# Performance work log

Hardware: AMD Instinct MI355X
Metric: run time of the kernel (lower is better)

Reference implementation:

```python
import jax, jax.numpy as jnp
import numpy as np

K_CONV = 4
NUM_HEADS = 16
NUM_KV_HEADS = 8
D_HEAD = 128
ROPE_THETA = 10000.0
EPS = 1e-6
NEG_INF = -1e30


def canon_b(x, w):
    """Canon-B: causal depthwise conv1d (kernel K_CONV) with residual.
    x: [B, S, C], w: [C, K_CONV]. out[t] = x[t] + sum_k w[:,k] * x[t-k]."""
    S = x.shape[1]
    xp = jnp.pad(x, ((0, 0), (K_CONV - 1, 0), (0, 0)))
    conv = sum(xp[:, K_CONV - 1 - k:K_CONV - 1 - k + S, :] * w[:, k] for k in range(K_CONV))
    return x + conv


def rms_norm(x, w):
    var = jnp.mean(x * x, axis=-1, keepdims=True)
    return x * jax.lax.rsqrt(var + EPS) * w


def rope_cos_sin(S, d):
    inv_freq = 1.0 / (ROPE_THETA ** (jnp.arange(0, d, 2, dtype=jnp.float32) / d))
    freqs = jnp.arange(S, dtype=jnp.float32)[:, None] * inv_freq  # [S, d/2]
    emb = jnp.concatenate([freqs, freqs], axis=-1)  # [S, d]
    return jnp.cos(emb), jnp.sin(emb)


def rotate_half(x):
    x1, x2 = jnp.split(x, 2, axis=-1)
    return jnp.concatenate([-x2, x1], axis=-1)


def setup_inputs() -> dict:
    key = jax.random.key(0)
    ks = jax.random.split(key, 8)
    B, S, D = 2, 2048, 2048
    Dkv = NUM_KV_HEADS * D_HEAD
    s = 0.02
    return {
        "hidden_states": jax.random.normal(ks[0], (B, S, D), jnp.float32),
        "Wq": jax.random.normal(ks[1], (D, D), jnp.float32) * s,
        "Wk": jax.random.normal(ks[2], (Dkv, D), jnp.float32) * s,
        "Wv": jax.random.normal(ks[3], (Dkv, D), jnp.float32) * s,
        "Wo": jax.random.normal(ks[4], (D, D), jnp.float32) * s,
        "canon_q_w": jax.random.normal(ks[5], (D, K_CONV), jnp.float32) * 0.1,
        "canon_k_w": jax.random.normal(ks[6], (Dkv, K_CONV), jnp.float32) * 0.1,
        "canon_v_w": jax.random.normal(ks[7], (Dkv, K_CONV), jnp.float32) * 0.1,
        "q_norm_w": jnp.ones((D_HEAD,), jnp.float32),
        "k_norm_w": jnp.ones((D_HEAD,), jnp.float32),
    }


def reference(hidden_states, Wq, Wk, Wv, Wo, canon_q_w, canon_k_w, canon_v_w, q_norm_w, k_norm_w):
    B, S, D = hidden_states.shape
    scale = 1.0 / np.sqrt(D_HEAD)
    groups = NUM_HEADS // NUM_KV_HEADS

    # QKV projections (no bias)
    q = hidden_states @ Wq.T
    k = hidden_states @ Wk.T
    v = hidden_states @ Wv.T

    # Canon-B causal depthwise conv on flat projections
    q = canon_b(q, canon_q_w)
    k = canon_b(k, canon_k_w)
    v = canon_b(v, canon_v_w)

    # Split heads: [B, S, H, d_head]
    q = q.reshape(B, S, NUM_HEADS, D_HEAD)
    k = k.reshape(B, S, NUM_KV_HEADS, D_HEAD)
    v = v.reshape(B, S, NUM_KV_HEADS, D_HEAD)

    # qk RMSNorm over d_head
    q = rms_norm(q, q_norm_w)
    k = rms_norm(k, k_norm_w)

    # RoPE
    cos, sin = rope_cos_sin(S, D_HEAD)  # [S, d_head]
    cos = cos[None, :, None, :]
    sin = sin[None, :, None, :]
    q = q * cos + rotate_half(q) * sin
    k = k * cos + rotate_half(k) * sin

    # [B, H, S, d_head]
    q = q.transpose(0, 2, 1, 3)
    k = k.transpose(0, 2, 1, 3)
    v = v.transpose(0, 2, 1, 3)

    # GQA: repeat kv heads
    k = jnp.repeat(k, groups, axis=1)
    v = jnp.repeat(v, groups, axis=1)

    # Causal attention (eager)
    scores = jnp.einsum("bhqd,bhkd->bhqk", q, k) * scale
    causal = jnp.tril(jnp.ones((S, S), bool))
    scores = jnp.where(causal, scores, NEG_INF)
    probs = jax.nn.softmax(scores, axis=-1)
    attn = jnp.einsum("bhqk,bhkd->bhqd", probs, v)

    out = attn.transpose(0, 2, 1, 3).reshape(B, S, D)
    return out @ Wo.T
```

## Files before the change

### kernel.cpp

```cpp
#include <hip/hip_runtime.h>
#include <hip/hip_bf16.h>

typedef __bf16 bf16;
typedef __bf16 bf16x8 __attribute__((ext_vector_type(8)));
typedef float  floatx4 __attribute__((ext_vector_type(4)));

#define AS1 __attribute__((address_space(1)))
#define AS3 __attribute__((address_space(3)))

#define B_    2
#define S_    2048
#define D_    2048
#define H_    16
#define KVH_  8
#define DH_   128
#define M_    4096
#define NQKV_ 4096

__global__ __launch_bounds__(256) void prep_kernel(const float* __restrict__ hidden,
                                                   const float* __restrict__ Wq,
                                                   const float* __restrict__ Wk,
                                                   const float* __restrict__ Wv,
                                                   const float* __restrict__ Wo,
                                                   bf16* __restrict__ X,
                                                   bf16* __restrict__ Wcat,
                                                   bf16* __restrict__ Wob,
                                                   float* __restrict__ cost,
                                                   float* __restrict__ sint) {
    size_t u = (size_t)blockIdx.x * 256 + threadIdx.x;
    if (u < 5242880) {
        const float* src; bf16* dst; size_t off;
        if (u < 2097152)      { src = hidden; dst = X;              off = u; }
        else if (u < 3145728) { src = Wq;     dst = Wcat;           off = u - 2097152; }
        else if (u < 3670016) { src = Wk;     dst = Wcat + 4194304; off = u - 3145728; }
        else if (u < 4194304) { src = Wv;     dst = Wcat + 6291456; off = u - 3670016; }
        else                  { src = Wo;     dst = Wob;            off = u - 4194304; }
        float4 v = *(const float4*)(src + off * 4);
        union { bf16 h[4]; double d; } uu;
        uu.h[0] = (bf16)v.x; uu.h[1] = (bf16)v.y; uu.h[2] = (bf16)v.z; uu.h[3] = (bf16)v.w;
        *(double*)(dst + off * 4) = uu.d;
    } else {
        int r = (int)(u - 5242880);
        int t = r >> 6, fi = r & 63;
        float inv = expf(-9.210340371976184f * (float)fi * (1.0f / 64.0f));
        float ang = (float)t * inv;
        cost[r] = cosf(ang);
        sint[r] = sinf(ang);
    }
}

#define BM 128
#define BN 128
#define BK 64
template <typename CT>
__global__ __launch_bounds__(256) void gemm_bt(const bf16* __restrict__ A,
                                               const bf16* __restrict__ Bw,
                                               CT* __restrict__ C,
                                               int M, int N, int K) {
    __shared__ __align__(16) bf16 Als[BM * BK];
    __shared__ __align__(16) bf16 Bls[BN * BK];
    int tid  = threadIdx.x;
    int wave = tid >> 6, lane = tid & 63;
    int quad = lane >> 4, l16 = lane & 15;
    int wm = (wave >> 1) << 6;
    int wn = (wave & 1) << 6;

    long bm0 = (long)blockIdx.y * BM;
    long bn0 = (long)blockIdx.x * BN;
    const bf16* Ab = A  + bm0 * K;
    const bf16* Bb = Bw + bn0 * K;

    int srow = wave * 32 + (lane >> 3);
    int scol = ((lane & 7) ^ (lane >> 3)) << 3;
    int sdst = (wave * 32 + (lane >> 3)) * BK + ((lane & 7) << 3);

    floatx4 acc[4][4] = {};

    for (int k0 = 0; k0 < K; k0 += BK) {
        #pragma unroll
        for (int i = 0; i < 4; ++i) {
            const bf16* ga = Ab + (long)(srow + i * 8) * K + k0 + scol;
            const bf16* gb = Bb + (long)(srow + i * 8) * K + k0 + scol;
            __builtin_amdgcn_global_load_lds((AS1 const unsigned int*)ga,
                                             (AS3 unsigned int*)(Als + sdst + i * 512), 16, 0, 0);
            __builtin_amdgcn_global_load_lds((AS1 const unsigned int*)gb,
                                             (AS3 unsigned int*)(Bls + sdst + i * 512), 16, 0, 0);
        }
        __syncthreads();
        #pragma unroll
        for (int ks = 0; ks < 2; ++ks) {
            bf16x8 af[4], bfr[4];
            #pragma unroll
            for (int t = 0; t < 4; ++t) {
                int row = wm + t * 16 + l16;
                int g = (ks * 4 + quad) ^ (row & 7);
                af[t] = *(const bf16x8*)(Als + row * BK + (g << 3));
            }
            #pragma unroll
            for (int t = 0; t < 4; ++t) {
                int row = wn + t * 16 + l16;
                int g = (ks * 4 + quad) ^ (row & 7);
                bfr[t] = *(const bf16x8*)(Bls + row * BK + (g << 3));
            }
            #pragma unroll
            for (int mt = 0; mt < 4; ++mt)
                #pragma unroll
                for (int nt = 0; nt < 4; ++nt)
                    acc[mt][nt] = __builtin_amdgcn_mfma_f32_16x16x32_bf16(af[mt], bfr[nt], acc[mt][nt], 0, 0, 0);
        }
        __syncthreads();
    }
    #pragma unroll
    for (int mt = 0; mt < 4; ++mt) {
        #pragma unroll
        for (int nt = 0; nt < 4; ++nt) {
            long row = bm0 + wm + mt * 16 + quad * 4;
            long col = bn0 + wn + nt * 16 + l16;
            #pragma unroll
            for (int r = 0; r < 4; ++r)
                C[(row + r) * N + col] = (CT)acc[mt][nt][r];
        }
    }
}

__global__ __launch_bounds__(256, 4) void canon_kernel(const bf16* __restrict__ QKV,
                                                       const float* __restrict__ wq,
                                                       const float* __restrict__ wk,
                                                       const float* __restrict__ wv,
                                                       const float* __restrict__ qnw,
                                                       const float* __restrict__ knw,
                                                       const float* __restrict__ cost,
                                                       const float* __restrict__ sint,
                                                       bf16* __restrict__ qf,
                                                       bf16* __restrict__ kf,
                                                       bf16* __restrict__ vfrag) {
    __shared__ __align__(16) bf16 vtile[32 * 520];
    int tid  = threadIdx.x;
    int wid  = blockIdx.x * 4 + (tid >> 6);
    int lane = tid & 63;
    int b  = wid >> 11;
    int g  = (wid >> 8) & 7;
    int c  = wid & 255;
    int t0 = c << 3;
    int ch = (g << 9) + (lane << 3);

    const float* wrow; int cw;
    if (g < 4)      { wrow = wq; cw = ch; }
    else if (g < 6) { wrow = wk; cw = ch - 2048; }
    else            { wrow = wv; cw = ch - 3072; }

    float4 w4[8];
    #pragma unroll
    for (int j = 0; j < 8; ++j) w4[j] = *(const float4*)(wrow + (cw + j) * 4);

    union U8 { float4 v; bf16 h[8]; };
    const bf16* srcb = QKV + (size_t)((b << 11) + t0) * 4096 + ch;

    float xm1[8], xm2[8], xm3[8];
    if (t0 > 0) {
        U8 u1, u2, u3;
        u1.v = *(const float4*)(srcb - 4096);
        u2.v = *(const float4*)(srcb - 2 * 4096);
        u3.v = *(const float4*)(srcb - 3 * 4096);
        #pragma unroll
        for (int i = 0; i < 8; ++i) {
            xm1[i] = (float)u1.h[i]; xm2[i] = (float)u2.h[i]; xm3[i] = (float)u3.h[i];
        }
    } else {
        #pragma unroll
        for (int i = 0; i < 8; ++i) { xm1[i] = 0.f; xm2[i] = 0.f; xm3[i] = 0.f; }
    }

    float4 nxtv = *(const float4*)(srcb);

    if (g < 6) {
        int j0   = ch & 127;
        int head = (g < 4) ? (ch >> 7) : ((ch - 2048) >> 7);
        const float* nw = (g < 4) ? qnw : knw;
        float nwv[8];
        {
            float4 na = *(const float4*)(nw + j0);
            float4 nb = *(const float4*)(nw + j0 + 4);
            #pragma unroll
            for (int i = 0; i < 8; ++i) nwv[i] = (i < 4) ? (&na.x)[i] : (&nb.x)[i - 4];
        }
        int ks = (lane >> 2) & 3, qd = lane & 3;
        size_t qkbase = ((size_t)((g < 4 ? (b << 4) : (b << 3)) + head) << 18)
                      + ((size_t)(t0 >> 4) << 11) + ((size_t)ks << 9)
                      + ((size_t)qd << 7) + ((size_t)(t0 & 15) << 3);
        bf16* dstb = (g < 4 ? qf : kf) + qkbase;

        int fi0 = j0 & 63;
        bool neg = (j0 < 64);
        const float* ctp = cost + t0 * 64 + fi0;
        const float* stp = sint + t0 * 64 + fi0;

        #pragma unroll
        for (int tt = 0; tt < 8; ++tt) {
            U8 u; u.v = nxtv;
            if (tt < 7) nxtv = *(const float4*)(srcb + (size_t)(tt + 1) * 4096);
            float cur[8], cv[8];
            #pragma unroll
            for (int i = 0; i < 8; ++i) cur[i] = (float)u.h[i];
            #pragma unroll
            for (int i = 0; i < 8; ++i) {
                float a = fmaf(w4[i].x, cur[i], cur[i]);
                a = fmaf(w4[i].y, xm1[i], a);
                a = fmaf(w4[i].z, xm2[i], a);
                cv[i] = fmaf(w4[i].w, xm3[i], a);
                xm3[i] = xm2[i]; xm2[i] = xm1[i]; xm1[i] = cur[i];
            }
            float ss = 0.f;
            #pragma unroll
            for (int i = 0; i < 8; ++i) ss = fmaf(cv[i], cv[i], ss);
            ss += __shfl_xor(ss, 1); ss += __shfl_xor(ss, 2);
            ss += __shfl_xor(ss, 4); ss += __shfl_xor(ss, 8);
            float r1 = rsqrtf(ss * (1.0f / 128.0f) + 1e-6f);
            float xn[8];
            #pragma unroll
            for (int i = 0; i < 8; ++i) xn[i] = cv[i] * r1 * nwv[i];
            float4 ca = *(const float4*)(ctp + tt * 64);
            float4 cb = *(const float4*)(ctp + tt * 64 + 4);
            float4 sa = *(const float4*)(stp + tt * 64);
            float4 sb = *(const float4*)(stp + tt * 64 + 4);
            __align__(16) bf16 outv[8];
            #pragma unroll
            for (int i = 0; i < 8; ++i) {
                float xp  = __shfl_xor(xn[i], 8);
                float rot = neg ? -xp : xp;
                float cc = (i < 4) ? (&ca.x)[i] : (&cb.x)[i - 4];
                float sn = (i < 4) ? (&sa.x)[i] : (&sb.x)[i - 4];
                outv[i] = (bf16)fmaf(xn[i], cc, rot * sn);
            }
            *(float4*)(dstb + (tt << 3)) = *(const float4*)outv;
        }
    } else {
        int lrow0 = (tid >> 6) << 3;
        #pragma unroll
        for (int tt = 0; tt < 8; ++tt) {
            U8 u; u.v = nxtv;
            if (tt < 7) nxtv = *(const float4*)(srcb + (size_t)(tt + 1) * 4096);
            float cur[8];
            __align__(16) bf16 outv[8];
            #pragma unroll
            for (int i = 0; i < 8; ++i) cur[i] = (float)u.h[i];
            #pragma unroll
            for (int i = 0; i < 8; ++i) {
                float a = fmaf(w4[i].x, cur[i], cur[i]);
                a = fmaf(w4[i].y, xm1[i], a);
                a = fmaf(w4[i].z, xm2[i], a);
                a = fmaf(w4[i].w, xm3[i], a);
                xm3[i] = xm2[i]; xm2[i] = xm1[i]; xm1[i] = cur[i];
                outv[i] = (bf16)a;
            }
            *(float4*)(&vtile[(lrow0 + tt) * 520 + (lane << 3)]) = *(const float4*)outv;
        }
        __syncthreads();
        int T  = (((blockIdx.x * 4) & 255) << 3);
        int kt = T >> 6, ks = (T >> 5) & 1;
        int hb = (g - 6) << 2;
        #pragma unroll
        for (int p = 0; p < 8; ++p) {
            int cidx = tid + p * 256;
            int hd  = cidx >> 9;
            int dnt = (cidx >> 6) & 7;
            int lc  = cidx & 63;
            int quad = lc >> 4, l16 = lc & 15;
            int scol = hd * 128 + dnt * 16 + l16;
            __align__(16) bf16 outv[8];
            #pragma unroll
            for (int j = 0; j < 8; ++j)
                outv[j] = vtile[(quad * 8 + j) * 520 + scol];
            size_t off = (((size_t)(b * 8 + hb + hd) * 32 + kt) << 13)
                       + ((size_t)ks << 12) + ((size_t)dnt << 9) + ((size_t)lc << 3);
            *(float4*)(vfrag + off) = *(const float4*)outv;
        }
    }
}

__global__ __launch_bounds__(256) void flash_attn(const bf16* __restrict__ qf,
                                                  const bf16* __restrict__ kf,
                                                  const bf16* __restrict__ vfrag,
                                                  bf16* __restrict__ attn) {
    __shared__ __align__(16) bf16 Kls[2][8192];
    __shared__ __align__(16) bf16 Vls[2][8192];
    __shared__ __align__(16) bf16 Pls[4][16][72];
    int lid  = blockIdx.x;
    int pair = lid & 15;
    int b    = pair >> 3, kvh = pair & 7;
    int inner = lid >> 4;
    int qt   = 31 - (inner >> 1);
    int h    = kvh * 2 + (inner & 1);
    int tid = threadIdx.x, wave = tid >> 6, lane = tid & 63;
    int quad = lane >> 4, l16 = lane & 15;
    int qrow0 = (qt << 6) + (wave << 4);

    const bf16* kfp = kf    + (((size_t)b * KVH_ + kvh) << 18);
    const bf16* vfp = vfrag + (((size_t)b * KVH_ + kvh) << 18);
    const bf16* qfp = qf    + ((((size_t)(b * H_ + h) * 128 + (qt << 2) + wave)) << 11);

    bf16x8 aq[4];
    #pragma unroll
    for (int ks = 0; ks < 4; ++ks)
        aq[ks] = *(const bf16x8*)(qfp + (ks << 9) + (lane << 3));

    floatx4 o[8] = {};
    float l_i[4] = {0.f, 0.f, 0.f, 0.f};
    const float scl2 = 0.08838834764831845f * 1.4426950408889634f;

    int ktiles = qt + 1;
    int eo = tid << 3;

    #pragma unroll
    for (int i = 0; i < 4; ++i) {
        __builtin_amdgcn_global_load_lds((AS1 const unsigned int*)(kfp + eo + (i << 11)),
                                         (AS3 unsigned int*)(&Kls[0][0] + eo + (i << 11)), 16, 0, 0);
        __builtin_amdgcn_global_load_lds((AS1 const unsigned int*)(vfp + eo + (i << 11)),
                                         (AS3 unsigned int*)(&Vls[0][0] + eo + (i << 11)), 16, 0, 0);
    }

    int cur = 0;
    for (int kt = 0; kt < ktiles; ++kt) {
        __syncthreads();
        if (kt + 1 < ktiles) {
            const bf16* ksrc = kfp + (((size_t)(kt + 1)) << 13) + eo;
            const bf16* vsrc = vfp + (((size_t)(kt + 1)) << 13) + eo;
            bf16* kd = &Kls[cur ^ 1][0] + eo;
            bf16* vd = &Vls[cur ^ 1][0] + eo;
            #pragma unroll
            for (int i = 0; i < 4; ++i) {
                __builtin_amdgcn_global_load_lds((AS1 const unsigned int*)(ksrc + (i << 11)),
                                                 (AS3 unsigned int*)(kd + (i << 11)), 16, 0, 0);
                __builtin_amdgcn_global_load_lds((AS1 const unsigned int*)(vsrc + (i << 11)),
                                                 (AS3 unsigned int*)(vd + (i << 11)), 16, 0, 0);
            }
        }
        const bf16* Kb = &Kls[cur][0];
        const bf16* Vb = &Vls[cur][0];
        floatx4 sc[4] = {};
        #pragma unroll
        for (int nt = 0; nt < 4; ++nt) {
            #pragma unroll
            for (int ks = 0; ks < 4; ++ks) {
                bf16x8 kb8 = *(const bf16x8*)(Kb + ((nt * 4 + ks) << 9) + (lane << 3));
                sc[nt] = __builtin_amdgcn_mfma_f32_16x16x32_bf16(aq[ks], kb8, sc[nt], 0, 0, 0);
            }
        }
        int qr0 = qrow0 + (quad << 2);
        int kb = kt << 6;
        if (kt == ktiles - 1) {
            #pragma unroll
            for (int nt = 0; nt < 4; ++nt) {
                int key = kb + nt * 16 + l16;
                #pragma unroll
                for (int r = 0; r < 4; ++r) {
                    float pv = exp2f(sc[nt][r] * scl2);
                    pv = (key <= qr0 + r) ? pv : 0.f;
                    l_i[r] += pv;
                    Pls[wave][(quad << 2) + r][nt * 16 + l16] = (bf16)pv;
                }
            }
        } else {
            #pragma unroll
            for (int nt = 0; nt < 4; ++nt) {
                #pragma unroll
                for (int r = 0; r < 4; ++r) {
                    float pv = exp2f(sc[nt][r] * scl2);
                    l_i[r] += pv;
                    Pls[wave][(quad << 2) + r][nt * 16 + l16] = (bf16)pv;
                }
            }
        }
        {
            bf16x8 pa = *(const bf16x8*)(&Pls[wave][l16][(quad << 3)]);
            #pragma unroll
            for (int dnt = 0; dnt < 8; ++dnt) {
                bf16x8 vb = *(const bf16x8*)(Vb + ((size_t)dnt << 9) + (lane << 3));
                o[dnt] = __builtin_amdgcn_mfma_f32_16x16x32_bf16(pa, vb, o[dnt], 0, 0, 0);
            }
            bf16x8 pb = *(const bf16x8*)(&Pls[wave][l16][32 + (quad << 3)]);
            #pragma unroll
            for (int dnt = 0; dnt < 8; ++dnt) {
                bf16x8 vb = *(const bf16x8*)(Vb + ((size_t)(8 + dnt) << 9) + (lane << 3));
                o[dnt] = __builtin_amdgcn_mfma_f32_16x16x32_bf16(pb, vb, o[dnt], 0, 0, 0);
            }
        }
        cur ^= 1;
    }
    #pragma unroll
    for (int r = 0; r < 4; ++r) {
        float l = l_i[r];
        l += __shfl_xor(l, 1); l += __shfl_xor(l, 2);
        l += __shfl_xor(l, 4); l += __shfl_xor(l, 8);
        l_i[r] = 1.0f / l;
    }
    #pragma unroll
    for (int dnt = 0; dnt < 8; ++dnt) {
        #pragma unroll
        for (int r = 0; r < 4; ++r) {
            size_t row = (size_t)b * S_ + qrow0 + (quad << 2) + r;
            attn[row * D_ + h * DH_ + dnt * 16 + l16] = (bf16)(o[dnt][r] * l_i[r]);
        }
    }
}

extern "C" void kernel_launch(void* const* d_in, const int* in_sizes, int n_in,
                              void* d_out, int out_size, void* d_ws, size_t ws_size,
                              hipStream_t stream) {
    const float* hidden = (const float*)d_in[0];
    const float* Wq  = (const float*)d_in[1];
    const float* Wk  = (const float*)d_in[2];
    const float* Wv  = (const float*)d_in[3];
    const float* Wo  = (const float*)d_in[4];
    const float* cqw = (const float*)d_in[5];
    const float* ckw = (const float*)d_in[6];
    const float* cvw = (const float*)d_in[7];
    const float* qnw = (const float*)d_in[8];
    const float* knw = (const float*)d_in[9];

    char* p = (char*)d_ws;
    auto alloc = [&](size_t bytes) { char* r = p; p += (bytes + 255) & ~(size_t)255; return r; };
    bf16*  X    = (bf16*)alloc((size_t)M_ * D_ * 2);
    bf16*  Wcat = (bf16*)alloc((size_t)NQKV_ * D_ * 2);
    bf16*  Wob  = (bf16*)alloc((size_t)D_ * D_ * 2);
    bf16*  QKV  = (bf16*)alloc((size_t)M_ * NQKV_ * 2);
    bf16*  qfb  = (bf16*)alloc((size_t)B_ * H_ * S_ * DH_ * 2);
    bf16*  kfb  = (bf16*)alloc((size_t)B_ * KVH_ * S_ * DH_ * 2);
    bf16*  vfr  = (bf16*)alloc((size_t)B_ * KVH_ * S_ * DH_ * 2);
    float* cost = (float*)alloc((size_t)S_ * 64 * 4);
    float* sint = (float*)alloc((size_t)S_ * 64 * 4);
    bf16*  attnb = QKV;

    prep_kernel<<<20992, 256, 0, stream>>>(hidden, Wq, Wk, Wv, Wo, X, Wcat, Wob, cost, sint);
    gemm_bt<bf16><<<dim3(NQKV_ / BN, M_ / BM), 256, 0, stream>>>(X, Wcat, QKV, M_, NQKV_, D_);
    canon_kernel<<<1024, 256, 0, stream>>>(QKV, cqw, ckw, cvw, qnw, knw, cost, sint, qfb, kfb, vfr);
    flash_attn<<<1024, 256, 0, stream>>>(qfb, kfb, vfr, attnb);
    gemm_bt<float><<<dim3(D_ / BN, M_ / BM), 256, 0, stream>>>(attnb, Wob, (float*)d_out, M_, D_, D_);
}
```

Measured before the change: 377.5 us.

## Use 256x256-tile 8-wave pipelined GEMM for the fused QKV projection

Adds a new bf16 GEMM kernel with 256x256 output tiles and 512 threads (8 waves, each computing 128x64). It uses a 4-stage LDS ring filled by direct global-to-LDS loads with swizzled chunks, split A/B staging interleaved with two MFMA half-phases, setprio around the MFMA blocks, and an XCD-aware block remap. It replaces the 128x128 GEMM for the QKV projection only, aiming for more reuse per byte loaded and better latency hiding. The cost is higher register pressure from 32 accumulators per lane and reliance on exact vmcnt accounting, which is fragile.

```diff
diff --git a/kernel.cpp b/kernel.cpp
--- a/kernel.cpp
+++ b/kernel.cpp
@@ -49,6 +49,112 @@
     }
 }
 
+__global__ __launch_bounds__(512, 2) void gemm_bt8(const bf16* __restrict__ A,
+                                                   const bf16* __restrict__ Bw,
+                                                   bf16* __restrict__ C,
+                                                   int M, int N, int K) {
+    __shared__ __align__(16) bf16 Als[4][256 * 32];
+    __shared__ __align__(16) bf16 Bls[4][256 * 32];
+    int tid  = threadIdx.x;
+    int wave = tid >> 6, lane = tid & 63;
+    int quad = lane >> 4, l16 = lane & 15;
+    int wr = wave >> 2, wc = wave & 3;
+
+    int nbx = N >> 8;
+    int wg  = (blockIdx.x & 7) * ((int)gridDim.x >> 3) + (blockIdx.x >> 3);
+    int by  = wg / nbx, bx = wg % nbx;
+    long bm0 = (long)by << 8, bn0 = (long)bx << 8;
+
+    int slot8 = ((quad ^ ((l16 ^ (l16 >> 2)) & 3)) << 3);
+
+    int srow   = tid >> 2;
+    int schunk = (tid & 3) ^ ((srow ^ (srow >> 2)) & 3);
+    const bf16* Asrc = A  + (bm0 + srow) * K + schunk * 8;
+    const bf16* Bsrc = Bw + (bn0 + srow) * K + schunk * 8;
+    size_t ldoff = (size_t)128 * K;
+
+    floatx4 acc[8][4] = {};
+    int NT = K >> 5;
+
+#define STAGE_A8(t) { int d_ = (t) & 3; long k0_ = (long)(t) << 5;                                   \
+    __builtin_amdgcn_global_load_lds((AS1 const unsigned int*)(Asrc + k0_),                          \
+                                     (AS3 unsigned int*)(&Als[d_][0] + tid * 8), 16, 0, 0);          \
+    __builtin_amdgcn_global_load_lds((AS1 const unsigned int*)(Asrc + ldoff + k0_),                  \
+                                     (AS3 unsigned int*)(&Als[d_][0] + tid * 8 + 4096), 16, 0, 0); }
+#define STAGE_B8(t) { int d_ = (t) & 3; long k0_ = (long)(t) << 5;                                   \
+    __builtin_amdgcn_global_load_lds((AS1 const unsigned int*)(Bsrc + k0_),                          \
+                                     (AS3 unsigned int*)(&Bls[d_][0] + tid * 8), 16, 0, 0);          \
+    __builtin_amdgcn_global_load_lds((AS1 const unsigned int*)(Bsrc + ldoff + k0_),                  \
+                                     (AS3 unsigned int*)(&Bls[d_][0] + tid * 8 + 4096), 16, 0, 0); }
+
+    STAGE_A8(0); STAGE_B8(0);
+    STAGE_A8(1); STAGE_B8(1);
+    STAGE_A8(2); STAGE_B8(2);
+    asm volatile("s_waitcnt vmcnt(8)" ::: "memory");
+    __builtin_amdgcn_s_barrier();
+
+    for (int u = 0; u < NT; ++u) {
+        const bf16* Ab = &Als[u & 3][0];
+        const bf16* Bb = &Bls[u & 3][0];
+        bf16x8 af[4], bfr[4];
+        #pragma unroll
+        for (int mt = 0; mt < 4; ++mt) {
+            int row = wr * 128 + mt * 16 + l16;
+            af[mt] = *(const bf16x8*)(Ab + row * 32 + slot8);
+        }
+        #pragma unroll
+        for (int nt = 0; nt < 4; ++nt) {
+            int col = wc * 64 + nt * 16 + l16;
+            bfr[nt] = *(const bf16x8*)(Bb + col * 32 + slot8);
+        }
+        if (u + 3 < NT) { STAGE_A8(u + 3); }
+        __builtin_amdgcn_s_barrier();
+        asm volatile("s_waitcnt lgkmcnt(0)" ::: "memory");
+        __builtin_amdgcn_sched_barrier(0);
+        __builtin_amdgcn_s_setprio(1);
+        #pragma unroll
+        for (int mt = 0; mt < 4; ++mt)
+            #pragma unroll
+            for (int nt = 0; nt < 4; ++nt)
+                acc[mt][nt] = __builtin_amdgcn_mfma_f32_16x16x32_bf16(af[mt], bfr[nt], acc[mt][nt], 0, 0, 0);
+        __builtin_amdgcn_s_setprio(0);
+        __builtin_amdgcn_s_barrier();
+        #pragma unroll
+        for (int mt = 0; mt < 4; ++mt) {
+            int row = wr * 128 + 64 + mt * 16 + l16;
+            af[mt] = *(const bf16x8*)(Ab + row * 32 + slot8);
+        }
+        if (u + 3 < NT) { STAGE_B8(u + 3); }
+        if (u < NT - 3)       { asm volatile("s_waitcnt vmcnt(8)" ::: "memory"); }
+        else if (u == NT - 3) { asm volatile("s_waitcnt vmcnt(4)" ::: "memory"); }
+        else                  { asm volatile("s_waitcnt vmcnt(0)" ::: "memory"); }
+        __builtin_amdgcn_s_barrier();
+        asm volatile("s_waitcnt lgkmcnt(0)" ::: "memory");
+        __builtin_amdgcn_sched_barrier(0);
+        __builtin_amdgcn_s_setprio(1);
+        #pragma unroll
+        for (int mt = 0; mt < 4; ++mt)
+            #pragma unroll
+            for (int nt = 0; nt < 4; ++nt)
+                acc[4 + mt][nt] = __builtin_amdgcn_mfma_f32_16x16x32_bf16(af[mt], bfr[nt], acc[4 + mt][nt], 0, 0, 0);
+        __builtin_amdgcn_s_setprio(0);
+        __builtin_amdgcn_s_barrier();
+    }
+#undef STAGE_A8
+#undef STAGE_B8
+    #pragma unroll
+    for (int am = 0; am < 8; ++am) {
+        #pragma unroll
+        for (int nt = 0; nt < 4; ++nt) {
+            long row = bm0 + wr * 128 + (am >> 2) * 64 + (am & 3) * 16 + quad * 4;
+            long col = bn0 + wc * 64 + nt * 16 + l16;
+            #pragma unroll
+            for (int r = 0; r < 4; ++r)
+                C[(row + r) * N + col] = (bf16)acc[am][nt][r];
+        }
+    }
+}
+
 #define BM 128
 #define BN 128
 #define BK 64
@@ -432,7 +538,7 @@
     bf16*  attnb = QKV;
 
     prep_kernel<<<20992, 256, 0, stream>>>(hidden, Wq, Wk, Wv, Wo, X, Wcat, Wob, cost, sint);
-    gemm_bt<bf16><<<dim3(NQKV_ / BN, M_ / BM), 256, 0, stream>>>(X, Wcat, QKV, M_, NQKV_, D_);
+    gemm_bt8<<<(M_ / 256) * (NQKV_ / 256), 512, 0, stream>>>(X, Wcat, QKV, M_, NQKV_, D_);
     canon_kernel<<<1024, 256, 0, stream>>>(QKV, cqw, ckw, cvw, qnw, knw, cost, sint, qfb, kfb, vfr);
     flash_attn<<<1024, 256, 0, stream>>>(qfb, kfb, vfr, attnb);
     gemm_bt<float><<<dim3(D_ / BN, M_ / BM), 256, 0, stream>>>(attnb, Wob, (float*)d_out, M_, D_, D_);
```

Result: faster. 353.9 us (-6.2%).
